# Optimization experiments

Measured on AMD Instinct MI355X. Metric: run time of the kernel, lower is better.

## Reference

```python
import jax, jax.numpy as jnp
import numpy as np

B = 4096
N_QUBITS = 4
N_LAYERS = 3
C64 = jnp.complex64


def setup_inputs() -> dict:
    key = jax.random.key(0)
    ks = jax.random.split(key, 14)
    f = jax.random.normal
    return {
        "x": f(ks[0], (B, 1, 28, 28), jnp.float32),
        "qparams": f(ks[1], (N_LAYERS, N_QUBITS, 3), jnp.float32),
        "dw4_w": f(ks[2], (4, 1, 4, 4), jnp.float32) * 0.1,
        "dw4_b": f(ks[3], (4,), jnp.float32) * 0.1,
        "pw4_w": f(ks[4], (4, 4, 1, 1), jnp.float32) * 0.3,
        "pw4_b": f(ks[5], (4,), jnp.float32) * 0.1,
        "dw8_w": f(ks[6], (4, 1, 8, 8), jnp.float32) * 0.05,
        "dw8_b": f(ks[7], (4,), jnp.float32) * 0.1,
        "pw8_w": f(ks[8], (4, 4, 1, 1), jnp.float32) * 0.3,
        "pw8_b": f(ks[9], (4,), jnp.float32) * 0.1,
        "res_w": f(ks[10], (4, 1, 1, 1), jnp.float32) * 0.3,
        "res_b": f(ks[11], (4,), jnp.float32) * 0.1,
        "head_w": f(ks[12], (10, 4 * 3 * 14 * 14), jnp.float32) * 0.02,
        "head_b": f(ks[13], (10,), jnp.float32) * 0.02,
    }


def _rx(t):
    c = jnp.cos(t / 2).astype(C64)
    s = (-1j * jnp.sin(t / 2)).astype(C64)
    return jnp.stack([jnp.stack([c, s]), jnp.stack([s, c])])


def _ry(t):
    c = jnp.cos(t / 2)
    s = jnp.sin(t / 2)
    return jnp.stack([jnp.stack([c, -s]), jnp.stack([s, c])]).astype(C64)


def _rz(t):
    z = jnp.zeros((), C64)
    return jnp.stack([jnp.stack([jnp.exp(-0.5j * t).astype(C64), z]),
                      jnp.stack([z, jnp.exp(0.5j * t).astype(C64)])])


def _apply_1q(state, U, wire):
    # state: (n,2,2,2,2); U: (2,2) shared across patches
    st = jnp.moveaxis(state, wire + 1, -1)
    st = jnp.einsum('ij,n...j->n...i', U, st)
    return jnp.moveaxis(st, -1, wire + 1)


def _apply_1q_batched(state, U, wire):
    # U: (n,2,2), one gate per patch (input encoding)
    st = jnp.moveaxis(state, wire + 1, -1)
    st = jnp.einsum('nij,n...j->n...i', U, st)
    return jnp.moveaxis(st, -1, wire + 1)


def _cnot(state, c, t):
    a, b = jnp.split(state, 2, axis=c + 1)
    return jnp.concatenate([a, jnp.flip(b, axis=t + 1)], axis=c + 1)


def _quantum_features(patches, params):
    # patches: (n,4) angles; returns (n,4) PauliZ expectations
    n = patches.shape[0]
    state = jnp.zeros((n, 16), C64).at[:, 0].set(1.0).reshape(n, 2, 2, 2, 2)
    c = jnp.cos(patches / 2)
    s = jnp.sin(patches / 2)
    for q in range(N_QUBITS):
        Uq = jnp.stack([jnp.stack([c[:, q], -s[:, q]], -1),
                        jnp.stack([s[:, q], c[:, q]], -1)], -2).astype(C64)
        state = _apply_1q_batched(state, Uq, q)
    for l in range(N_LAYERS):
        for q in range(N_QUBITS):
            state = _apply_1q(state, _rx(params[l, q, 0]), q)
            state = _apply_1q(state, _ry(params[l, q, 1]), q)
            state = _apply_1q(state, _rz(params[l, q, 2]), q)
        for q in range(N_QUBITS - 1):
            state = _cnot(state, q, q + 1)
        state = _cnot(state, N_QUBITS - 1, 0)
    probs = jnp.real(state * jnp.conj(state))  # (n,2,2,2,2)
    ez = [jnp.sum(jnp.take(probs, 0, axis=q + 1) - jnp.take(probs, 1, axis=q + 1),
                  axis=(1, 2, 3)) for q in range(N_QUBITS)]
    return jnp.stack(ez, -1).astype(jnp.float32)


def _conv(x, w, b, stride):
    y = jax.lax.conv_general_dilated(x, w, (stride, stride), 'VALID',
                                     dimension_numbers=('NCHW', 'OIHW', 'NCHW'))
    return y + b[None, :, None, None]


def _forward(x, qparams, dw4_w, dw4_b, pw4_w, pw4_b, dw8_w, dw8_b, pw8_w, pw8_b,
             res_w, res_b, head_w, head_b):
    b = x.shape[0]
    # residual branch: 1x1 conv then 2x2 avg-pool down to the 14x14 grid
    res = _conv(x, res_w, res_b, 1)                      # (B,4,28,28)
    res = res.reshape(b, 4, 14, 2, 14, 2).mean(axis=(3, 5))  # (B,4,14,14)
    # quantum branch over non-overlapping 2x2 patches
    patches = x[:, 0].reshape(b, 14, 2, 14, 2).transpose(0, 1, 3, 2, 4)
    patches = patches.reshape(b * 14 * 14, 4)
    feat2 = _quantum_features(patches, qparams).reshape(b, 14, 14, 4)
    # multi-scale conv branches, upsampled (nearest) to the 14x14 grid
    feat4 = jax.nn.relu(_conv(_conv(x, dw4_w, dw4_b, 4), pw4_w, pw4_b, 1))  # (B,4,7,7)
    feat4 = jnp.repeat(jnp.repeat(feat4, 2, axis=2), 2, axis=3)             # (B,4,14,14)
    feat8 = jax.nn.relu(_conv(_conv(x, dw8_w, dw8_b, 8), pw8_w, pw8_b, 1))  # (B,4,3,3)
    feat8 = jax.image.resize(feat8, (b, 4, 14, 14), 'nearest')
    f4 = jnp.transpose(feat4, (0, 2, 3, 1))
    f8 = jnp.transpose(feat8, (0, 2, 3, 1))
    r = jnp.transpose(res, (0, 2, 3, 1))
    out = jnp.concatenate([feat2, f4, f8], axis=3) + jnp.tile(r, (1, 1, 1, 3))
    logits = out.reshape(b, -1) @ head_w.T + head_b
    return jax.nn.log_softmax(logits, axis=-1)


def reference(x, qparams, dw4_w, dw4_b, pw4_w, pw4_b, dw8_w, dw8_b, pw8_w, pw8_b,
              res_w, res_b, head_w, head_b):
    return _forward(x, qparams, dw4_w, dw4_b, pw4_w, pw4_b, dw8_w, dw8_b,
                    pw8_w, pw8_b, res_w, res_b, head_w, head_b)
```

## Files before the change

### kernel.cpp

```cpp
#include <hip/hip_runtime.h>

#define WS_T    0
#define WS_HQ   512
#define WS_WA   8352
#define WS_H4   10312
#define WS_H8   12272
#define WS_C10  12632

__device__ __forceinline__ float4 f4fma(const float4 a, const float s, const float4 c) {
  return {fmaf(a.x, s, c.x), fmaf(a.y, s, c.y), fmaf(a.z, s, c.z), fmaf(a.w, s, c.w)};
}
__device__ __forceinline__ float4 f4add(const float4 a, const float4 b) {
  return {a.x + b.x, a.y + b.y, a.z + b.z, a.w + b.w};
}

__global__ __launch_bounds__(256) void prep_kernel(
    const float* __restrict__ qp, const float* __restrict__ hw,
    const float* __restrict__ res_w, const float* __restrict__ res_b,
    const float* __restrict__ hb, float* __restrict__ ws) {
  __shared__ float row[2352];
  __shared__ float cred[4];
  __shared__ float Sr[16][16];
  __shared__ float Si[16][16];
  __shared__ float csc[36], css[36];
  __shared__ float Afs[256][4];
  const int t = threadIdx.x;

  if (blockIdx.x < 10) {
    const int k = blockIdx.x;
    for (int i = t; i < 2352; i += 256) row[i] = hw[k * 2352 + i];
    __syncthreads();
    float cpart = 0.f;
    if (t < 196) {
      const int b12 = t * 12;
      float4 h = {row[b12], row[b12 + 1], row[b12 + 2], row[b12 + 3]};
      ((float4*)(ws + WS_HQ))[k * 196 + t] = h;
      float wa = 0.f;
#pragma unroll
      for (int c = 0; c < 4; ++c) {
        const float s3 = row[b12 + c] + row[b12 + 4 + c] + row[b12 + 8 + c];
        wa += res_w[c] * s3;
        cpart += res_b[c] * s3;
      }
      ws[WS_WA + k * 196 + t] = wa;
    }
    if (t < 49) {
      const int i4 = t / 7, j4 = t % 7;
      float4 s = {0.f, 0.f, 0.f, 0.f};
#pragma unroll
      for (int di = 0; di < 2; ++di)
#pragma unroll
        for (int dj = 0; dj < 2; ++dj) {
          const int pos = (2 * i4 + di) * 14 + 2 * j4 + dj;
          s.x += row[pos * 12 + 4]; s.y += row[pos * 12 + 5];
          s.z += row[pos * 12 + 6]; s.w += row[pos * 12 + 7];
        }
      ((float4*)(ws + WS_H4))[k * 49 + t] = s;
    }
    if (t < 9) {
      const int i8 = t / 3, j8 = t % 3;
      const int pi0 = (i8 == 0) ? 0 : ((i8 == 1) ? 5 : 9);
      const int pi1 = (i8 == 0) ? 5 : ((i8 == 1) ? 9 : 14);
      const int pj0 = (j8 == 0) ? 0 : ((j8 == 1) ? 5 : 9);
      const int pj1 = (j8 == 0) ? 5 : ((j8 == 1) ? 9 : 14);
      float4 s = {0.f, 0.f, 0.f, 0.f};
      for (int pi = pi0; pi < pi1; ++pi)
        for (int pj = pj0; pj < pj1; ++pj) {
          const int pos = pi * 14 + pj;
          s.x += row[pos * 12 + 8]; s.y += row[pos * 12 + 9];
          s.z += row[pos * 12 + 10]; s.w += row[pos * 12 + 11];
        }
      ((float4*)(ws + WS_H8))[k * 9 + t] = s;
    }
#pragma unroll
    for (int off = 32; off > 0; off >>= 1) cpart += __shfl_xor(cpart, off);
    if ((t & 63) == 0) cred[t >> 6] = cpart;
    __syncthreads();
    if (t == 0) ws[WS_C10 + k] = hb[k] + cred[0] + cred[1] + cred[2] + cred[3];
    return;
  }

  if (t < 36) {
    float th = 0.5f * qp[t];
    csc[t] = cosf(th);
    css[t] = sinf(th);
  }
  Sr[t >> 4][t & 15] = ((t >> 4) == (t & 15)) ? 1.f : 0.f;
  Si[t >> 4][t & 15] = 0.f;
  __syncthreads();

  const int col = t >> 3, pp = t & 7;
  for (int l = 0; l < 3; ++l) {
    for (int q = 0; q < 4; ++q) {
      const int m = 8 >> q;
      for (int r = 0; r < 3; ++r) {
        if (t < 128) {
          const float c = csc[l * 12 + q * 3 + r];
          const float s = css[l * 12 + q * 3 + r];
          const int k = ((pp & ~(m - 1)) << 1) | (pp & (m - 1));
          const int k1 = k | m;
          float a0r = Sr[col][k],  a0i = Si[col][k];
          float a1r = Sr[col][k1], a1i = Si[col][k1];
          float n0r, n0i, n1r, n1i;
          if (r == 0) {
            n0r = c * a0r + s * a1i;  n0i = c * a0i - s * a1r;
            n1r = c * a1r + s * a0i;  n1i = c * a1i - s * a0r;
          } else if (r == 1) {
            n0r = c * a0r - s * a1r;  n0i = c * a0i - s * a1i;
            n1r = s * a0r + c * a1r;  n1i = s * a0i + c * a1i;
          } else {
            n0r = c * a0r + s * a0i;  n0i = c * a0i - s * a0r;
            n1r = c * a1r - s * a1i;  n1i = c * a1i + s * a1r;
          }
          Sr[col][k] = n0r;  Si[col][k] = n0i;
          Sr[col][k1] = n1r; Si[col][k1] = n1i;
        }
        __syncthreads();
      }
    }
    for (int e = 0; e < 4; ++e) {
      if (t < 64) {
        const int c2 = t >> 2, p2 = t & 3;
        const int mc = 8 >> e;
        const int mt = 8 >> ((e + 1) & 3);
        const int rest = 15 & ~(mc | mt);
        const int rl = rest & (-rest);
        const int rh = rest ^ rl;
        const int k = mc | ((p2 & 1) ? rl : 0) | ((p2 & 2) ? rh : 0);
        const int k1 = k | mt;
        float tr = Sr[c2][k]; Sr[c2][k] = Sr[c2][k1]; Sr[c2][k1] = tr;
        float ti = Si[c2][k]; Si[c2][k] = Si[c2][k1]; Si[c2][k1] = ti;
      }
      __syncthreads();
    }
  }

  {
    const int i = t >> 4, j = t & 15;
    float a0 = 0.f, a1 = 0.f, a2 = 0.f, a3 = 0.f;
    for (int k = 0; k < 16; ++k) {
      float pr = Sr[i][k] * Sr[j][k] + Si[i][k] * Si[j][k];
      a0 += (k & 8) ? -pr : pr;
      a1 += (k & 4) ? -pr : pr;
      a2 += (k & 2) ? -pr : pr;
      a3 += (k & 1) ? -pr : pr;
    }
    Afs[t][0] = a0; Afs[t][1] = a1; Afs[t][2] = a2; Afs[t][3] = a3;
  }
  __syncthreads();

  for (int o = t; o < 324; o += 256) {
    const int mi = o >> 2, q = o & 3;
    const int m0 = mi / 27, m1 = (mi / 9) % 3, m2 = (mi / 3) % 3, m3 = mi % 3;
    const int mm[4] = {m0, m1, m2, m3};
    float acc = 0.f;
    for (int c = 0; c < 16; ++c) {
      int ii = 0, jj = 0; float sg = 1.f;
      for (int qb = 0; qb < 4; ++qb) {
        const int cb = (c >> qb) & 1, bit = 8 >> qb, mq = mm[qb];
        if (mq == 2) { if (cb) ii |= bit; else jj |= bit; }
        else if (cb) { ii |= bit; jj |= bit; if (mq == 1) sg = -sg; }
      }
      acc += sg * Afs[ii * 16 + jj][q];
    }
    ws[WS_T + mi * 4 + q] = acc * 0.0625f;
  }
}

__global__ __launch_bounds__(256, 4) void qmain_kernel(
    const float* __restrict__ x, const float4* __restrict__ T4,
    const float4* __restrict__ HQ4, const float* __restrict__ WA,
    const float4* __restrict__ H44, const float4* __restrict__ H84,
    const float* __restrict__ C10,
    const float* __restrict__ dw4_w, const float* __restrict__ dw4_b,
    const float* __restrict__ pw4_w, const float* __restrict__ pw4_b,
    const float* __restrict__ dw8_w, const float* __restrict__ dw8_b,
    const float* __restrict__ pw8_w, const float* __restrict__ pw8_b,
    float* __restrict__ out) {
  __shared__ __align__(16) float xs[784];
  __shared__ float accs[10 * 257];
  __shared__ float part[160];
  __shared__ float lgs[10];
  const int b = blockIdx.x, t = threadIdx.x;
  const int rot = ((b >> 8) + b) & 3;
  const int vt = (t + (rot << 6)) & 255;
  const float4* xs4 = (const float4*)xs;

  if (t < 196) ((float4*)xs)[t] = ((const float4*)(x + b * 784))[t];
  __syncthreads();

  float acc[10];
#pragma unroll
  for (int k = 0; k < 10; ++k) acc[k] = 0.f;

  if (vt < 196) {
    const int pi = vt / 14, pj = vt % 14;
    const int base = (2 * pi) * 28 + 2 * pj;
    const float a0 = xs[base], a1 = xs[base + 1];
    const float a2 = xs[base + 28], a3 = xs[base + 29];
    float c0, s0, c1, s1, c2, s2, c3, s3;
    __sincosf(a0, &s0, &c0);
    __sincosf(a1, &s1, &c1);
    __sincosf(a2, &s2, &c2);
    __sincosf(a3, &s3, &c3);
    float4 ea = {0.f, 0.f, 0.f, 0.f};
    float4 eb = {0.f, 0.f, 0.f, 0.f};
    float4 ec = {0.f, 0.f, 0.f, 0.f};
#pragma unroll
    for (int g = 0; g < 9; ++g) {
      const float4 t0 = T4[g * 9 + 0], t1 = T4[g * 9 + 1], t2 = T4[g * 9 + 2];
      const float4 t3 = T4[g * 9 + 3], t4 = T4[g * 9 + 4], t5 = T4[g * 9 + 5];
      const float4 t6 = T4[g * 9 + 6], t7 = T4[g * 9 + 7], t8 = T4[g * 9 + 8];
      const float4 u0 = f4fma(t2, s3, f4fma(t1, c3, t0));
      const float4 u1 = f4fma(t5, s3, f4fma(t4, c3, t3));
      const float4 u2 = f4fma(t8, s3, f4fma(t7, c3, t6));
      float4 inner = f4fma(u2, s2, f4fma(u1, c2, u0));
      const int m1 = g % 3;
      if (m1 == 1) inner = {inner.x * c1, inner.y * c1, inner.z * c1, inner.w * c1};
      if (m1 == 2) inner = {inner.x * s1, inner.y * s1, inner.z * s1, inner.w * s1};
      if (g < 3)      ea = f4add(ea, inner);
      else if (g < 6) eb = f4add(eb, inner);
      else            ec = f4add(ec, inner);
    }
    const float4 e = f4fma(ec, s0, f4fma(eb, c0, ea));
    const float avg = 0.25f * (a0 + a1 + a2 + a3);
#pragma unroll
    for (int k = 0; k < 10; ++k) {
      const float4 h = HQ4[k * 196 + vt];
      float a = fmaf(h.x, e.x, fmaf(h.y, e.y, fmaf(h.z, e.z, h.w * e.w)));
      acc[k] = fmaf(WA[k * 196 + vt], avg, a);
    }
  } else {
    const int u = vt - 196;
    if (u < 36) {
      const int pos = u >> 2, ch = u & 3;
      const int i8 = pos / 3, j8 = pos % 3;
      const float4* w84 = (const float4*)dw8_w;
      float4 a8 = {0.f, 0.f, 0.f, 0.f};
#pragma unroll
      for (int uu = 0; uu < 8; ++uu) {
        const float4 xa = xs4[(8 * i8 + uu) * 7 + 2 * j8];
        const float4 xb = xs4[(8 * i8 + uu) * 7 + 2 * j8 + 1];
        const float4 wa = w84[ch * 16 + uu * 2];
        const float4 wb = w84[ch * 16 + uu * 2 + 1];
        a8.x = fmaf(wa.x, xa.x, a8.x); a8.y = fmaf(wa.y, xa.y, a8.y);
        a8.z = fmaf(wa.z, xa.z, a8.z); a8.w = fmaf(wa.w, xa.w, a8.w);
        a8.x = fmaf(wb.x, xb.x, a8.x); a8.y = fmaf(wb.y, xb.y, a8.y);
        a8.z = fmaf(wb.z, xb.z, a8.z); a8.w = fmaf(wb.w, xb.w, a8.w);
      }
      const float d8 = a8.x + a8.y + a8.z + a8.w + dw8_b[ch];
      const float z1 = __shfl_down(d8, 1);
      const float z2 = __shfl_down(d8, 2);
      const float z3 = __shfl_down(d8, 3);
      if (ch == 0) {
        const float yv[4] = {d8, z1, z2, z3};
        float z[4];
#pragma unroll
        for (int o = 0; o < 4; ++o) {
          float zz = pw8_b[o];
#pragma unroll
          for (int c = 0; c < 4; ++c) zz = fmaf(pw8_w[o * 4 + c], yv[c], zz);
          z[o] = fmaxf(zz, 0.f);
        }
#pragma unroll
        for (int k = 0; k < 10; ++k) {
          const float4 h = H84[k * 9 + pos];
          acc[k] += fmaf(h.x, z[0], fmaf(h.y, z[1], fmaf(h.z, z[2], h.w * z[3])));
        }
      }
    }
    if (u < 49) {
      const int i = u / 7, j = u % 7;
      const float4* w44 = (const float4*)dw4_w;
      float y[4];
#pragma unroll
      for (int c = 0; c < 4; ++c) {
        float4 a4 = {0.f, 0.f, 0.f, 0.f};
#pragma unroll
        for (int uu = 0; uu < 4; ++uu) {
          const float4 xa = xs4[(4 * i + uu) * 7 + j];
          const float4 wa = w44[c * 4 + uu];
          a4.x = fmaf(wa.x, xa.x, a4.x); a4.y = fmaf(wa.y, xa.y, a4.y);
          a4.z = fmaf(wa.z, xa.z, a4.z); a4.w = fmaf(wa.w, xa.w, a4.w);
        }
        y[c] = a4.x + a4.y + a4.z + a4.w + dw4_b[c];
      }
      float z[4];
#pragma unroll
      for (int o = 0; o < 4; ++o) {
        float zz = pw4_b[o];
#pragma unroll
        for (int c = 0; c < 4; ++c) zz = fmaf(pw4_w[o * 4 + c], y[c], zz);
        z[o] = fmaxf(zz, 0.f);
      }
#pragma unroll
      for (int k = 0; k < 10; ++k) {
        const float4 h = H44[k * 49 + u];
        acc[k] += fmaf(h.x, z[0], fmaf(h.y, z[1], fmaf(h.z, z[2], h.w * z[3])));
      }
    }
  }

#pragma unroll
  for (int k = 0; k < 10; ++k) accs[k * 257 + t] = acc[k];
  __syncthreads();
  if (t < 160) {
    const int k = t >> 4, c = t & 15;
    float s = 0.f;
#pragma unroll
    for (int i = 0; i < 16; ++i) s += accs[k * 257 + c + 16 * i];
    part[k * 16 + c] = s;
  }
  __syncthreads();
  if (t < 10) {
    float lg = C10[t];
#pragma unroll
    for (int c = 0; c < 16; ++c) lg += part[t * 16 + c];
    lgs[t] = lg;
  }
  __syncthreads();
  if (t < 10) {
    float m = lgs[0];
#pragma unroll
    for (int i = 1; i < 10; ++i) m = fmaxf(m, lgs[i]);
    float se = 0.f;
#pragma unroll
    for (int i = 0; i < 10; ++i) se += __expf(lgs[i] - m);
    out[b * 10 + t] = lgs[t] - m - __logf(se);
  }
}

extern "C" void kernel_launch(void* const* d_in, const int* in_sizes, int n_in,
                              void* d_out, int out_size, void* d_ws, size_t ws_size,
                              hipStream_t stream) {
  const float* x      = (const float*)d_in[0];
  const float* qp     = (const float*)d_in[1];
  const float* dw4_w  = (const float*)d_in[2];
  const float* dw4_b  = (const float*)d_in[3];
  const float* pw4_w  = (const float*)d_in[4];
  const float* pw4_b  = (const float*)d_in[5];
  const float* dw8_w  = (const float*)d_in[6];
  const float* dw8_b  = (const float*)d_in[7];
  const float* pw8_w  = (const float*)d_in[8];
  const float* pw8_b  = (const float*)d_in[9];
  const float* res_w  = (const float*)d_in[10];
  const float* res_b  = (const float*)d_in[11];
  const float* head_w = (const float*)d_in[12];
  const float* head_b = (const float*)d_in[13];
  float* out = (float*)d_out;
  float* ws = (float*)d_ws;
  const int B = in_sizes[0] / 784;

  hipLaunchKernelGGL(prep_kernel, dim3(11), dim3(256), 0, stream,
                     qp, head_w, res_w, res_b, head_b, ws);
  hipLaunchKernelGGL(qmain_kernel, dim3(B), dim3(256), 0, stream,
                     x, (const float4*)(ws + WS_T),
                     (const float4*)(ws + WS_HQ), ws + WS_WA,
                     (const float4*)(ws + WS_H4), (const float4*)(ws + WS_H8),
                     ws + WS_C10,
                     dw4_w, dw4_b, pw4_w, pw4_b, dw8_w, dw8_b, pw8_w, pw8_b,
                     out);
}
```

Before: 35.08 us.

## Map one wavefront per image with shuffle reductions instead of block-per-image

Restructures the main kernel so each 64-lane wavefront handles one whole image (four images per block), looping over patches instead of one block with 256 threads per image. The block-level shared-memory reduction and its barriers are replaced by wavefront xor-shuffle reductions and an in-register log-softmax. The 8x8 conv branch now computes all four channels per thread without cross-lane shuffles, and the quantum feature accumulation is folded into one weighted FMA chain. The change trades per-thread parallelism for fewer barriers and less shared memory traffic, and it adds a serial loop of four patch rounds per lane.

```diff
diff --git a/kernel.cpp b/kernel.cpp
--- a/kernel.cpp
+++ b/kernel.cpp
@@ -10,8 +10,11 @@
 __device__ __forceinline__ float4 f4fma(const float4 a, const float s, const float4 c) {
   return {fmaf(a.x, s, c.x), fmaf(a.y, s, c.y), fmaf(a.z, s, c.z), fmaf(a.w, s, c.w)};
 }
-__device__ __forceinline__ float4 f4add(const float4 a, const float4 b) {
-  return {a.x + b.x, a.y + b.y, a.z + b.z, a.w + b.w};
+__device__ __forceinline__ float4 f4fma4(const float4 a, const float4 b, const float4 c) {
+  return {fmaf(a.x, b.x, c.x), fmaf(a.y, b.y, c.y), fmaf(a.z, b.z, c.z), fmaf(a.w, b.w, c.w)};
+}
+__device__ __forceinline__ float hsum4(const float4 a) {
+  return a.x + a.y + a.z + a.w;
 }
 
 __global__ __launch_bounds__(256) void prep_kernel(
@@ -176,90 +179,127 @@
     const float* __restrict__ pw4_w, const float* __restrict__ pw4_b,
     const float* __restrict__ dw8_w, const float* __restrict__ dw8_b,
     const float* __restrict__ pw8_w, const float* __restrict__ pw8_b,
-    float* __restrict__ out) {
-  __shared__ __align__(16) float xs[784];
-  __shared__ float accs[10 * 257];
-  __shared__ float part[160];
-  __shared__ float lgs[10];
-  const int b = blockIdx.x, t = threadIdx.x;
-  const int rot = ((b >> 8) + b) & 3;
-  const int vt = (t + (rot << 6)) & 255;
-  const float4* xs4 = (const float4*)xs;
-
-  if (t < 196) ((float4*)xs)[t] = ((const float4*)(x + b * 784))[t];
+    float* __restrict__ out, const int B) {
+  __shared__ __align__(16) float xs[4 * 792];
+  const int t = threadIdx.x;
+  const int w = t >> 6, lane = t & 63;
+  const int img = blockIdx.x * 4 + w;
+  float* xw = xs + w * 792;
+  const float4* xw4 = (const float4*)xw;
+
+  if (img < B) {
+    const float4* xg = (const float4*)(x + img * 784);
+#pragma unroll
+    for (int it = 0; it < 4; ++it) {
+      const int idx = it * 64 + lane;
+      if (idx < 196) ((float4*)xw)[idx] = xg[idx];
+    }
+  }
   __syncthreads();
 
+  if (img >= B) return;
+
   float acc[10];
 #pragma unroll
   for (int k = 0; k < 10; ++k) acc[k] = 0.f;
 
-  if (vt < 196) {
-    const int pi = vt / 14, pj = vt % 14;
-    const int base = (2 * pi) * 28 + 2 * pj;
-    const float a0 = xs[base], a1 = xs[base + 1];
-    const float a2 = xs[base + 28], a3 = xs[base + 29];
-    float c0, s0, c1, s1, c2, s2, c3, s3;
-    __sincosf(a0, &s0, &c0);
-    __sincosf(a1, &s1, &c1);
-    __sincosf(a2, &s2, &c2);
-    __sincosf(a3, &s3, &c3);
-    float4 ea = {0.f, 0.f, 0.f, 0.f};
-    float4 eb = {0.f, 0.f, 0.f, 0.f};
-    float4 ec = {0.f, 0.f, 0.f, 0.f};
-#pragma unroll
-    for (int g = 0; g < 9; ++g) {
-      const float4 t0 = T4[g * 9 + 0], t1 = T4[g * 9 + 1], t2 = T4[g * 9 + 2];
-      const float4 t3 = T4[g * 9 + 3], t4 = T4[g * 9 + 4], t5 = T4[g * 9 + 5];
-      const float4 t6 = T4[g * 9 + 6], t7 = T4[g * 9 + 7], t8 = T4[g * 9 + 8];
-      const float4 u0 = f4fma(t2, s3, f4fma(t1, c3, t0));
-      const float4 u1 = f4fma(t5, s3, f4fma(t4, c3, t3));
-      const float4 u2 = f4fma(t8, s3, f4fma(t7, c3, t6));
-      float4 inner = f4fma(u2, s2, f4fma(u1, c2, u0));
-      const int m1 = g % 3;
-      if (m1 == 1) inner = {inner.x * c1, inner.y * c1, inner.z * c1, inner.w * c1};
-      if (m1 == 2) inner = {inner.x * s1, inner.y * s1, inner.z * s1, inner.w * s1};
-      if (g < 3)      ea = f4add(ea, inner);
-      else if (g < 6) eb = f4add(eb, inner);
-      else            ec = f4add(ec, inner);
-    }
-    const float4 e = f4fma(ec, s0, f4fma(eb, c0, ea));
-    const float avg = 0.25f * (a0 + a1 + a2 + a3);
-#pragma unroll
-    for (int k = 0; k < 10; ++k) {
-      const float4 h = HQ4[k * 196 + vt];
-      float a = fmaf(h.x, e.x, fmaf(h.y, e.y, fmaf(h.z, e.z, h.w * e.w)));
-      acc[k] = fmaf(WA[k * 196 + vt], avg, a);
-    }
-  } else {
-    const int u = vt - 196;
-    if (u < 36) {
-      const int pos = u >> 2, ch = u & 3;
-      const int i8 = pos / 3, j8 = pos % 3;
-      const float4* w84 = (const float4*)dw8_w;
-      float4 a8 = {0.f, 0.f, 0.f, 0.f};
-#pragma unroll
-      for (int uu = 0; uu < 8; ++uu) {
-        const float4 xa = xs4[(8 * i8 + uu) * 7 + 2 * j8];
-        const float4 xb = xs4[(8 * i8 + uu) * 7 + 2 * j8 + 1];
-        const float4 wa = w84[ch * 16 + uu * 2];
-        const float4 wb = w84[ch * 16 + uu * 2 + 1];
-        a8.x = fmaf(wa.x, xa.x, a8.x); a8.y = fmaf(wa.y, xa.y, a8.y);
-        a8.z = fmaf(wa.z, xa.z, a8.z); a8.w = fmaf(wa.w, xa.w, a8.w);
-        a8.x = fmaf(wb.x, xb.x, a8.x); a8.y = fmaf(wb.y, xb.y, a8.y);
-        a8.z = fmaf(wb.z, xb.z, a8.z); a8.w = fmaf(wb.w, xb.w, a8.w);
-      }
-      const float d8 = a8.x + a8.y + a8.z + a8.w + dw8_b[ch];
-      const float z1 = __shfl_down(d8, 1);
-      const float z2 = __shfl_down(d8, 2);
-      const float z3 = __shfl_down(d8, 3);
-      if (ch == 0) {
-        const float yv[4] = {d8, z1, z2, z3};
+#pragma unroll 1
+  for (int r = 0; r < 4; ++r) {
+    const int p = r * 64 + lane;
+    if (p < 196) {
+      const int pi = p / 14, pj = p % 14;
+      const int base = 56 * pi + 2 * pj;
+      const float2 a01 = *(const float2*)(xw + base);
+      const float2 a23 = *(const float2*)(xw + base + 28);
+      const float a0 = a01.x, a1 = a01.y, a2 = a23.x, a3 = a23.y;
+      float c0, s0, c1, s1, c2, s2, c3, s3;
+      __sincosf(a0, &s0, &c0);
+      __sincosf(a1, &s1, &c1);
+      __sincosf(a2, &s2, &c2);
+      __sincosf(a3, &s3, &c3);
+      const float w01[9] = {1.f, c1, s1, c0, c0 * c1, c0 * s1, s0, s0 * c1, s0 * s1};
+      float4 e = {0.f, 0.f, 0.f, 0.f};
+#pragma unroll
+      for (int g = 0; g < 9; ++g) {
+        const float4 t0 = T4[g * 9 + 0], t1 = T4[g * 9 + 1], t2 = T4[g * 9 + 2];
+        const float4 t3 = T4[g * 9 + 3], t4 = T4[g * 9 + 4], t5 = T4[g * 9 + 5];
+        const float4 t6 = T4[g * 9 + 6], t7 = T4[g * 9 + 7], t8 = T4[g * 9 + 8];
+        const float4 u0 = f4fma(t2, s3, f4fma(t1, c3, t0));
+        const float4 u1 = f4fma(t5, s3, f4fma(t4, c3, t3));
+        const float4 u2 = f4fma(t8, s3, f4fma(t7, c3, t6));
+        const float4 inner = f4fma(u2, s2, f4fma(u1, c2, u0));
+        e = f4fma(inner, w01[g], e);
+      }
+      const float avg = 0.25f * (a0 + a1 + a2 + a3);
+#pragma unroll
+      for (int k = 0; k < 10; ++k) {
+        const float4 h = HQ4[k * 196 + p];
+        acc[k] += fmaf(h.x, e.x, fmaf(h.y, e.y,
+                  fmaf(h.z, e.z, fmaf(h.w, e.w, WA[k * 196 + p] * avg))));
+      }
+    } else {
+      const int u = p - 196;
+      if (u < 49) {
+        const int i = u / 7, j = u % 7;
+        const float4* w44 = (const float4*)dw4_w;
+        float4 q0 = {0.f, 0.f, 0.f, 0.f}, q1 = q0, q2 = q0, q3 = q0;
+#pragma unroll
+        for (int uu = 0; uu < 4; ++uu) {
+          const float4 xa = xw4[(4 * i + uu) * 7 + j];
+          q0 = f4fma4(w44[0 + uu], xa, q0);
+          q1 = f4fma4(w44[4 + uu], xa, q1);
+          q2 = f4fma4(w44[8 + uu], xa, q2);
+          q3 = f4fma4(w44[12 + uu], xa, q3);
+        }
+        const float y0 = hsum4(q0) + dw4_b[0];
+        const float y1 = hsum4(q1) + dw4_b[1];
+        const float y2 = hsum4(q2) + dw4_b[2];
+        const float y3 = hsum4(q3) + dw4_b[3];
+        float z[4];
+#pragma unroll
+        for (int o = 0; o < 4; ++o) {
+          float zz = pw4_b[o];
+          zz = fmaf(pw4_w[o * 4 + 0], y0, zz);
+          zz = fmaf(pw4_w[o * 4 + 1], y1, zz);
+          zz = fmaf(pw4_w[o * 4 + 2], y2, zz);
+          zz = fmaf(pw4_w[o * 4 + 3], y3, zz);
+          z[o] = fmaxf(zz, 0.f);
+        }
+#pragma unroll
+        for (int k = 0; k < 10; ++k) {
+          const float4 h = H44[k * 49 + u];
+          acc[k] += fmaf(h.x, z[0], fmaf(h.y, z[1], fmaf(h.z, z[2], h.w * z[3])));
+        }
+      } else if (u < 58) {
+        const int pos = u - 49;
+        const int i8 = pos / 3, j8 = pos % 3;
+        const float4* w84 = (const float4*)dw8_w;
+        float4 e0 = {0.f, 0.f, 0.f, 0.f}, e1 = e0, e2 = e0, e3 = e0;
+#pragma unroll
+        for (int uu = 0; uu < 8; ++uu) {
+          const float4 xa = xw4[(8 * i8 + uu) * 7 + 2 * j8];
+          const float4 xb = xw4[(8 * i8 + uu) * 7 + 2 * j8 + 1];
+          e0 = f4fma4(w84[0 + uu * 2], xa, e0);
+          e0 = f4fma4(w84[1 + uu * 2], xb, e0);
+          e1 = f4fma4(w84[16 + uu * 2], xa, e1);
+          e1 = f4fma4(w84[17 + uu * 2], xb, e1);
+          e2 = f4fma4(w84[32 + uu * 2], xa, e2);
+          e2 = f4fma4(w84[33 + uu * 2], xb, e2);
+          e3 = f4fma4(w84[48 + uu * 2], xa, e3);
+          e3 = f4fma4(w84[49 + uu * 2], xb, e3);
+        }
+        const float d0 = hsum4(e0) + dw8_b[0];
+        const float d1 = hsum4(e1) + dw8_b[1];
+        const float d2 = hsum4(e2) + dw8_b[2];
+        const float d3 = hsum4(e3) + dw8_b[3];
         float z[4];
 #pragma unroll
         for (int o = 0; o < 4; ++o) {
           float zz = pw8_b[o];
-#pragma unroll
-          for (int c = 0; c < 4; ++c) zz = fmaf(pw8_w[o * 4 + c], yv[c], zz);
+          zz = fmaf(pw8_w[o * 4 + 0], d0, zz);
+          zz = fmaf(pw8_w[o * 4 + 1], d1, zz);
+          zz = fmaf(pw8_w[o * 4 + 2], d2, zz);
+          zz = fmaf(pw8_w[o * 4 + 3], d3, zz);
           z[o] = fmaxf(zz, 0.f);
         }
 #pragma unroll
@@ -269,64 +309,36 @@
         }
       }
     }
-    if (u < 49) {
-      const int i = u / 7, j = u % 7;
-      const float4* w44 = (const float4*)dw4_w;
-      float y[4];
-#pragma unroll
-      for (int c = 0; c < 4; ++c) {
-        float4 a4 = {0.f, 0.f, 0.f, 0.f};
-#pragma unroll
-        for (int uu = 0; uu < 4; ++uu) {
-          const float4 xa = xs4[(4 * i + uu) * 7 + j];
-          const float4 wa = w44[c * 4 + uu];
-          a4.x = fmaf(wa.x, xa.x, a4.x); a4.y = fmaf(wa.y, xa.y, a4.y);
-          a4.z = fmaf(wa.z, xa.z, a4.z); a4.w = fmaf(wa.w, xa.w, a4.w);
-        }
-        y[c] = a4.x + a4.y + a4.z + a4.w + dw4_b[c];
-      }
-      float z[4];
-#pragma unroll
-      for (int o = 0; o < 4; ++o) {
-        float zz = pw4_b[o];
-#pragma unroll
-        for (int c = 0; c < 4; ++c) zz = fmaf(pw4_w[o * 4 + c], y[c], zz);
-        z[o] = fmaxf(zz, 0.f);
-      }
-#pragma unroll
-      for (int k = 0; k < 10; ++k) {
-        const float4 h = H44[k * 49 + u];
-        acc[k] += fmaf(h.x, z[0], fmaf(h.y, z[1], fmaf(h.z, z[2], h.w * z[3])));
-      }
-    }
-  }
-
-#pragma unroll
-  for (int k = 0; k < 10; ++k) accs[k * 257 + t] = acc[k];
-  __syncthreads();
-  if (t < 160) {
-    const int k = t >> 4, c = t & 15;
-    float s = 0.f;
-#pragma unroll
-    for (int i = 0; i < 16; ++i) s += accs[k * 257 + c + 16 * i];
-    part[k * 16 + c] = s;
-  }
-  __syncthreads();
-  if (t < 10) {
-    float lg = C10[t];
-#pragma unroll
-    for (int c = 0; c < 16; ++c) lg += part[t * 16 + c];
-    lgs[t] = lg;
-  }
-  __syncthreads();
-  if (t < 10) {
-    float m = lgs[0];
-#pragma unroll
-    for (int i = 1; i < 10; ++i) m = fmaxf(m, lgs[i]);
-    float se = 0.f;
-#pragma unroll
-    for (int i = 0; i < 10; ++i) se += __expf(lgs[i] - m);
-    out[b * 10 + t] = lgs[t] - m - __logf(se);
+  }
+
+#pragma unroll
+  for (int k = 0; k < 10; ++k) {
+    float v = acc[k];
+    v += __shfl_xor(v, 1);
+    v += __shfl_xor(v, 2);
+    v += __shfl_xor(v, 4);
+    v += __shfl_xor(v, 8);
+    v += __shfl_xor(v, 16);
+    v += __shfl_xor(v, 32);
+    acc[k] = v;
+  }
+
+  float lg[10], m = -1e30f;
+#pragma unroll
+  for (int k = 0; k < 10; ++k) {
+    lg[k] = acc[k] + C10[k];
+    m = fmaxf(m, lg[k]);
+  }
+  float se = 0.f;
+#pragma unroll
+  for (int k = 0; k < 10; ++k) se += __expf(lg[k] - m);
+  const float ls = m + __logf(se);
+  if (lane < 10) {
+    float v = lg[0];
+#pragma unroll
+    for (int k = 1; k < 10; ++k)
+      if (lane == k) v = lg[k];
+    out[img * 10 + lane] = v - ls;
   }
 }
 
@@ -353,11 +365,11 @@
 
   hipLaunchKernelGGL(prep_kernel, dim3(11), dim3(256), 0, stream,
                      qp, head_w, res_w, res_b, head_b, ws);
-  hipLaunchKernelGGL(qmain_kernel, dim3(B), dim3(256), 0, stream,
+  hipLaunchKernelGGL(qmain_kernel, dim3((B + 3) / 4), dim3(256), 0, stream,
                      x, (const float4*)(ws + WS_T),
                      (const float4*)(ws + WS_HQ), ws + WS_WA,
                      (const float4*)(ws + WS_H4), (const float4*)(ws + WS_H8),
                      ws + WS_C10,
                      dw4_w, dw4_b, pw4_w, pw4_b, dw8_w, dw8_b, pw8_w, pw8_b,
-                     out);
-}
+                     out, B);
+}
```

Result: faster. 33.86 us (-3.5%).
